# Optimization experiments

Hardware: AMD Instinct MI355X
Metric: run time of the kernel (lower is better)

The kernel has to match this reference:

```python
import jax, jax.numpy as jnp
import numpy as np

EPS = 1e-12

def setup_inputs() -> dict:
    key = jax.random.key(0)
    k1, k2 = jax.random.split(key)
    N, L, C = 32768, 256, 64
    mu = jax.random.uniform(k1, (N, L), dtype=jnp.float32)
    leaf_scores = jax.random.normal(k2, (L, C), dtype=jnp.float32)
    return {"mu": mu, "leaf_scores": leaf_scores}

def reference(mu, leaf_scores):
    # log path probabilities, clamped for numerical safety: (N, L)
    log_mu = jnp.log(jnp.clip(mu, EPS, None))
    # per-leaf class log-probs: (L, C)
    logQ = jax.nn.log_softmax(leaf_scores, axis=1)
    # y[n,k] = logsumexp_l( log_mu[n,l] + logQ[l,k] )  -> (N, C)
    scores = log_mu[:, :, None] + logQ[None, :, :]  # (N, L, C)
    return jax.scipy.special.logsumexp(scores, axis=1)
```

## Files before the change

### kernel.cpp

```cpp
#include <hip/hip_runtime.h>
#include <math.h>

#define NN 32768
#define LL 256
#define CC 64
#define EPSV 1e-12f

__global__ __launch_bounds__(64) void softmax_rows_kernel(
    const float* __restrict__ scores, float* __restrict__ Q) {
    const int l = blockIdx.x;
    const int k = threadIdx.x;
    float v = scores[l * CC + k];
    float m = v;
    #pragma unroll
    for (int off = 32; off > 0; off >>= 1) m = fmaxf(m, __shfl_xor(m, off));
    float e = expf(v - m);
    float s = e;
    #pragma unroll
    for (int off = 32; off > 0; off >>= 1) s += __shfl_xor(s, off);
    Q[l * CC + k] = e / s;
}

#define BM 64
#define BK 64
#define LDW (BK + 4)

__global__ __launch_bounds__(256) void leaf_mix_kernel(
    const float* __restrict__ mu, const float* __restrict__ Q,
    float* __restrict__ out) {
    __shared__ float muS[BM * LDW];
    __shared__ float QS[BK * LDW];

    const int tid = threadIdx.x;
    const int tx = tid & 15;
    const int ty = tid >> 4;
    const int rowBase = blockIdx.x * BM;

    __align__(16) float acc[4][4] = {{0.f,0.f,0.f,0.f},{0.f,0.f,0.f,0.f},
                                     {0.f,0.f,0.f,0.f},{0.f,0.f,0.f,0.f}};

    for (int kb = 0; kb < LL; kb += BK) {
        #pragma unroll
        for (int j = 0; j < 4; ++j) {
            const int f = tid + 256 * j;
            const int r = f >> 4;
            const int c = f & 15;
            float4 v = *(const float4*)(mu + (size_t)(rowBase + r) * LL + kb + c * 4);
            v.x = fmaxf(v.x, EPSV); v.y = fmaxf(v.y, EPSV);
            v.z = fmaxf(v.z, EPSV); v.w = fmaxf(v.w, EPSV);
            *(float4*)(muS + r * LDW + c * 4) = v;
        }
        #pragma unroll
        for (int j = 0; j < 4; ++j) {
            const int f = tid + 256 * j;
            const int r = f >> 4;
            const int c = f & 15;
            *(float4*)(QS + r * LDW + c * 4) =
                *(const float4*)(Q + (size_t)(kb + r) * CC + c * 4);
        }
        __syncthreads();

        #pragma unroll
        for (int l = 0; l < BK; l += 4) {
            __align__(16) float qv[4][4];
            __align__(16) float mv[4][4];
            #pragma unroll
            for (int j = 0; j < 4; ++j)
                *(float4*)qv[j] = *(const float4*)(QS + (l + j) * LDW + tx * 4);
            #pragma unroll
            for (int i = 0; i < 4; ++i)
                *(float4*)mv[i] = *(const float4*)(muS + (ty * 4 + i) * LDW + l);
            #pragma unroll
            for (int i = 0; i < 4; ++i)
                #pragma unroll
                for (int j = 0; j < 4; ++j)
                    #pragma unroll
                    for (int c = 0; c < 4; ++c)
                        acc[i][c] += mv[i][j] * qv[j][c];
        }
        __syncthreads();
    }

    #pragma unroll
    for (int i = 0; i < 4; ++i) {
        float4 o;
        o.x = logf(acc[i][0]);
        o.y = logf(acc[i][1]);
        o.z = logf(acc[i][2]);
        o.w = logf(acc[i][3]);
        *(float4*)(out + (size_t)(rowBase + ty * 4 + i) * CC + tx * 4) = o;
    }
}

extern "C" void kernel_launch(void* const* d_in, const int* in_sizes, int n_in,
                              void* d_out, int out_size, void* d_ws, size_t ws_size,
                              hipStream_t stream) {
    const float* mu     = (const float*)d_in[0];
    const float* scores = (const float*)d_in[1];
    float* out = (float*)d_out;
    float* Q   = (float*)d_ws;

    softmax_rows_kernel<<<LL, 64, 0, stream>>>(scores, Q);
    leaf_mix_kernel<<<NN / BM, 256, 0, stream>>>(mu, Q, out);
}
```

Before: 90.26 us.

## Use split-bf16 MFMA for leaf mixing with pre-swizzled Q fragments

Result: slower. 104.6 us (+15.8%).

```diff
diff --git a/kernel.cpp b/kernel.cpp
--- a/kernel.cpp
+++ b/kernel.cpp
@@ -6,90 +6,118 @@
 #define CC 64
 #define EPSV 1e-12f
 
-__global__ __launch_bounds__(64) void softmax_rows_kernel(
-    const float* __restrict__ scores, float* __restrict__ Q) {
-    const int l = blockIdx.x;
-    const int k = threadIdx.x;
-    float v = scores[l * CC + k];
-    float m = v;
-    #pragma unroll
-    for (int off = 32; off > 0; off >>= 1) m = fmaxf(m, __shfl_xor(m, off));
-    float e = expf(v - m);
-    float s = e;
-    #pragma unroll
-    for (int off = 32; off > 0; off >>= 1) s += __shfl_xor(s, off);
-    Q[l * CC + k] = e / s;
+typedef __attribute__((ext_vector_type(8))) short short8;
+typedef __attribute__((ext_vector_type(4))) float f32x4;
+
+__device__ inline void bf16_split(float x, short& h, short& l) {
+    union { float f; unsigned u; } cv;
+    cv.f = x;
+    unsigned hu = cv.u & 0xffff0000u;
+    h = (short)(cv.u >> 16);
+    union { unsigned u; float f; } ch;
+    ch.u = hu;
+    float xl = x - ch.f;
+    union { float f; unsigned u; } cl;
+    cl.f = xl;
+    l = (short)(cl.u >> 16);
 }
 
-#define BM 64
-#define BK 64
-#define LDW (BK + 4)
+__global__ __launch_bounds__(64) void prep_kernel(
+    const float* __restrict__ scores, float* __restrict__ wsB) {
+    __shared__ float Qs[32][64];
+    const int s = blockIdx.x;
+    const int lane = threadIdx.x;
 
-__global__ __launch_bounds__(256) void leaf_mix_kernel(
-    const float* __restrict__ mu, const float* __restrict__ Q,
+    for (int r = 0; r < 32; ++r) {
+        float v = scores[(size_t)(s * 32 + r) * CC + lane];
+        float mx = v;
+        #pragma unroll
+        for (int off = 32; off > 0; off >>= 1) mx = fmaxf(mx, __shfl_xor(mx, off));
+        float e = expf(v - mx);
+        float sum = e;
+        #pragma unroll
+        for (int off = 32; off > 0; off >>= 1) sum += __shfl_xor(sum, off);
+        Qs[r][lane] = e / sum;
+    }
+    __syncthreads();
+
+    const int quad = lane >> 4;
+    const int n = lane & 15;
+    short8* wsB8 = (short8*)wsB;
+    #pragma unroll
+    for (int t = 0; t < 4; ++t) {
+        short8 hi, lo;
+        #pragma unroll
+        for (int j = 0; j < 8; ++j) {
+            short h, l;
+            bf16_split(Qs[quad * 8 + j][t * 16 + n], h, l);
+            hi[j] = h; lo[j] = l;
+        }
+        const int rgn = (s * 4 + t) * 2;
+        wsB8[(rgn + 0) * 64 + lane] = hi;
+        wsB8[(rgn + 1) * 64 + lane] = lo;
+    }
+}
+
+__global__ __launch_bounds__(256) void leaf_mix_mfma_kernel(
+    const float* __restrict__ mu, const float* __restrict__ wsB,
     float* __restrict__ out) {
-    __shared__ float muS[BM * LDW];
-    __shared__ float QS[BK * LDW];
+    __shared__ float Bs[16384];
 
     const int tid = threadIdx.x;
-    const int tx = tid & 15;
-    const int ty = tid >> 4;
-    const int rowBase = blockIdx.x * BM;
+    {
+        const float4* src = (const float4*)wsB;
+        float4* dst = (float4*)Bs;
+        #pragma unroll
+        for (int i = 0; i < 16; ++i) dst[tid + 256 * i] = src[tid + 256 * i];
+    }
+    __syncthreads();
 
-    __align__(16) float acc[4][4] = {{0.f,0.f,0.f,0.f},{0.f,0.f,0.f,0.f},
-                                     {0.f,0.f,0.f,0.f},{0.f,0.f,0.f,0.f}};
+    const int wid = tid >> 6;
+    const int lane = tid & 63;
+    const int quad = lane >> 4;
+    const int m = lane & 15;
 
-    for (int kb = 0; kb < LL; kb += BK) {
+    const size_t row = (size_t)blockIdx.x * 64 + wid * 16 + m;
+    const float* arow = mu + row * LL + quad * 8;
+
+    float4 a[16];
+    #pragma unroll
+    for (int s = 0; s < 8; ++s) {
+        a[2 * s]     = *(const float4*)(arow + s * 32);
+        a[2 * s + 1] = *(const float4*)(arow + s * 32 + 4);
+    }
+
+    f32x4 acc[4] = {{0.f, 0.f, 0.f, 0.f}, {0.f, 0.f, 0.f, 0.f},
+                    {0.f, 0.f, 0.f, 0.f}, {0.f, 0.f, 0.f, 0.f}};
+
+    #pragma unroll
+    for (int s = 0; s < 8; ++s) {
+        float f[8] = {a[2 * s].x, a[2 * s].y, a[2 * s].z, a[2 * s].w,
+                      a[2 * s + 1].x, a[2 * s + 1].y, a[2 * s + 1].z, a[2 * s + 1].w};
+        short8 ahi, alo;
         #pragma unroll
-        for (int j = 0; j < 4; ++j) {
-            const int f = tid + 256 * j;
-            const int r = f >> 4;
-            const int c = f & 15;
-            float4 v = *(const float4*)(mu + (size_t)(rowBase + r) * LL + kb + c * 4);
-            v.x = fmaxf(v.x, EPSV); v.y = fmaxf(v.y, EPSV);
-            v.z = fmaxf(v.z, EPSV); v.w = fmaxf(v.w, EPSV);
-            *(float4*)(muS + r * LDW + c * 4) = v;
+        for (int e = 0; e < 8; ++e) {
+            short h, l;
+            bf16_split(fmaxf(f[e], EPSV), h, l);
+            ahi[e] = h; alo[e] = l;
         }
         #pragma unroll
-        for (int j = 0; j < 4; ++j) {
-            const int f = tid + 256 * j;
-            const int r = f >> 4;
-            const int c = f & 15;
-            *(float4*)(QS + r * LDW + c * 4) =
-                *(const float4*)(Q + (size_t)(kb + r) * CC + c * 4);
+        for (int t = 0; t < 4; ++t) {
+            const short8 bhi = ((const short8*)(Bs + (s * 4 + t) * 512))[lane];
+            const short8 blo = ((const short8*)(Bs + (s * 4 + t) * 512 + 256))[lane];
+            acc[t] = __builtin_amdgcn_mfma_f32_16x16x32_bf16(ahi, bhi, acc[t], 0, 0, 0);
+            acc[t] = __builtin_amdgcn_mfma_f32_16x16x32_bf16(alo, bhi, acc[t], 0, 0, 0);
+            acc[t] = __builtin_amdgcn_mfma_f32_16x16x32_bf16(ahi, blo, acc[t], 0, 0, 0);
         }
-        __syncthreads();
-
-        #pragma unroll
-        for (int l = 0; l < BK; l += 4) {
-            __align__(16) float qv[4][4];
-            __align__(16) float mv[4][4];
-            #pragma unroll
-            for (int j = 0; j < 4; ++j)
-                *(float4*)qv[j] = *(const float4*)(QS + (l + j) * LDW + tx * 4);
-            #pragma unroll
-            for (int i = 0; i < 4; ++i)
-                *(float4*)mv[i] = *(const float4*)(muS + (ty * 4 + i) * LDW + l);
-            #pragma unroll
-            for (int i = 0; i < 4; ++i)
-                #pragma unroll
-                for (int j = 0; j < 4; ++j)
-                    #pragma unroll
-                    for (int c = 0; c < 4; ++c)
-                        acc[i][c] += mv[i][j] * qv[j][c];
-        }
-        __syncthreads();
     }
 
+    const size_t outRow0 = (size_t)blockIdx.x * 64 + wid * 16 + quad * 4;
     #pragma unroll
-    for (int i = 0; i < 4; ++i) {
-        float4 o;
-        o.x = logf(acc[i][0]);
-        o.y = logf(acc[i][1]);
-        o.z = logf(acc[i][2]);
-        o.w = logf(acc[i][3]);
-        *(float4*)(out + (size_t)(rowBase + ty * 4 + i) * CC + tx * 4) = o;
-    }
+    for (int t = 0; t < 4; ++t)
+        #pragma unroll
+        for (int r = 0; r < 4; ++r)
+            out[(outRow0 + r) * CC + t * 16 + m] = logf(acc[t][r]);
 }
 
 extern "C" void kernel_launch(void* const* d_in, const int* in_sizes, int n_in,
@@ -98,8 +126,8 @@
     const float* mu     = (const float*)d_in[0];
     const float* scores = (const float*)d_in[1];
     float* out = (float*)d_out;
-    float* Q   = (float*)d_ws;
+    float* wsB = (float*)d_ws;
 
-    softmax_rows_kernel<<<LL, 64, 0, stream>>>(scores, Q);
-    leaf_mix_kernel<<<NN / BM, 256, 0, stream>>>(mu, Q, out);
+    prep_kernel<<<8, 64, 0, stream>>>(scores, wsB);
+    leaf_mix_mfma_kernel<<<NN / 64, 256, 0, stream>>>(mu, wsB, out);
 }
```
